# Optimization experiments

Measured on AMD Instinct MI355X. Metric: run time of the kernel, lower is better.

## Reference

```python
import jax, jax.numpy as jnp
import numpy as np
import math

FEATURE_DIMS = 6
D_HIDDEN = 32
N_TOKENS = 2097152
NUM_SEGMENTS = 8192
SCALE = 400.0 / math.log(10.0)


def setup_inputs() -> dict:
    key = jax.random.key(0)
    ks = jax.random.split(key, 8)
    x = jax.random.normal(ks[0], (N_TOKENS, FEATURE_DIMS), dtype=jnp.float32)
    segment_ids = jnp.sort(jax.random.randint(ks[1], (N_TOKENS,), 0, NUM_SEGMENTS)).astype(jnp.int32)
    # params (kaiming-ish init, same layout as nn.Linear: y = x @ W.T + b -> stored pre-transposed)
    W1 = jax.random.normal(ks[2], (FEATURE_DIMS, D_HIDDEN), dtype=jnp.float32) / np.sqrt(FEATURE_DIMS)
    b1 = jax.random.normal(ks[3], (D_HIDDEN,), dtype=jnp.float32) * 0.01
    wr = jax.random.normal(ks[4], (D_HIDDEN,), dtype=jnp.float32) / np.sqrt(D_HIDDEN)
    br = jax.random.normal(ks[5], (), dtype=jnp.float32) * 0.01
    wz = jax.random.normal(ks[6], (D_HIDDEN,), dtype=jnp.float32) / np.sqrt(D_HIDDEN)
    bz = jax.random.normal(ks[7], (), dtype=jnp.float32) * 0.01
    return {"x": x, "W1": W1, "b1": b1, "wr": wr, "br": br, "wz": wz, "bz": bz,
            "segment_ids": segment_ids, "num_segments": NUM_SEGMENTS}


def reference(x, W1, b1, wr, br, wz, bz, segment_ids, num_segments):
    # layer1: Linear + ReLU  -> h [N, d_hidden]
    h = jax.nn.relu(x @ W1 + b1)
    # rating / weight heads, squeezed to [N]
    r = h @ wr + br
    z = h @ wz + bz
    # per-segment (per-game) softmax over z, weighted sum of r -- single pass, no Python loop
    zmax = jax.ops.segment_max(z, segment_ids, num_segments=num_segments)  # [G], -inf for empty
    e = jnp.exp(z - zmax[segment_ids])                                      # [N]
    num = jax.ops.segment_sum(e * r, segment_ids, num_segments=num_segments)  # [G]
    den = jax.ops.segment_sum(e, segment_ids, num_segments=num_segments)      # [G]
    den_safe = jnp.where(den > 0, den, 1.0)
    preds = jnp.where(den > 0, num / den_safe, 0.0)  # empty segment -> 0, as in the torch code
    return SCALE * preds
```

## Files before the change

### kernel.cpp

```cpp
#include <hip/hip_runtime.h>

#define SCALE_F 173.71779276130078f
#define BLOCK 256
#define TPT 2
#define TOK_PER_BLOCK (BLOCK * TPT)

typedef float v2f __attribute__((ext_vector_type(2)));

__global__ void zero_ws_kernel(float* __restrict__ ws, int n) {
    int i = blockIdx.x * 256 + threadIdx.x;
    if (i < n) ws[i] = 0.0f;
}

__device__ __forceinline__ int swz(int q) { return q ^ ((q >> 3) & 7); }

__global__ __launch_bounds__(BLOCK, 8) void strength_main_kernel(
    const float* __restrict__ x,
    const float* __restrict__ W1,
    const float* __restrict__ b1,
    const float* __restrict__ wr,
    const float* __restrict__ brp,
    const float* __restrict__ wz,
    const float* __restrict__ bzp,
    const int*   __restrict__ seg,
    int N,
    float* __restrict__ num,
    float* __restrict__ den)
{
    __shared__ float4 xs[TOK_PER_BLOCK * 6 / 4];

    const int tid    = threadIdx.x;
    const int lane   = tid & 63;
    const int bstart = blockIdx.x * TOK_PER_BLOCK;
    const int t0     = bstart + tid * TPT;

    float a[TPT * 6];
    int   sg[TPT];
    int   kmax;

    if (bstart + TOK_PER_BLOCK <= N) {
        kmax = TPT;
        const float4* xg = (const float4*)(x + (size_t)bstart * 6);
        #pragma unroll
        for (int i = 0; i < 3; ++i) {
            int q = tid + BLOCK * i;
            xs[swz(q)] = xg[q];
        }
        __syncthreads();
        float4 v0 = xs[swz(3 * tid + 0)];
        float4 v1 = xs[swz(3 * tid + 1)];
        float4 v2 = xs[swz(3 * tid + 2)];
        a[0] = v0.x; a[1]  = v0.y; a[2]  = v0.z; a[3]  = v0.w;
        a[4] = v1.x; a[5]  = v1.y; a[6]  = v1.z; a[7]  = v1.w;
        a[8] = v2.x; a[9]  = v2.y; a[10] = v2.z; a[11] = v2.w;
        int2 s2 = *(const int2*)(seg + t0);
        sg[0] = s2.x; sg[1] = s2.y;
    } else {
        kmax = (t0 >= N) ? 0 : ((N - t0 < TPT) ? (N - t0) : TPT);
        #pragma unroll
        for (int k = 0; k < TPT; ++k) {
            if (k < kmax) {
                const float* xp = x + (size_t)(t0 + k) * 6;
                #pragma unroll
                for (int i = 0; i < 6; ++i) a[k * 6 + i] = xp[i];
                sg[k] = seg[t0 + k];
            } else {
                #pragma unroll
                for (int i = 0; i < 6; ++i) a[k * 6 + i] = 0.0f;
                sg[k] = -1;
            }
        }
    }

    v2f X[6];
    #pragma unroll
    for (int f = 0; f < 6; ++f) X[f] = (v2f){ a[f], a[6 + f] };

    const float brv = *brp;
    const float bzv = *bzp;

    v2f R = (v2f){brv, brv};
    v2f Z = (v2f){bzv, bzv};

    #pragma unroll 2
    for (int c = 0; c < 16; ++c) {
        const float2 w0 = *(const float2*)&W1[0 * 32 + 2 * c];
        const float2 w1 = *(const float2*)&W1[1 * 32 + 2 * c];
        const float2 w2 = *(const float2*)&W1[2 * 32 + 2 * c];
        const float2 w3 = *(const float2*)&W1[3 * 32 + 2 * c];
        const float2 w4 = *(const float2*)&W1[4 * 32 + 2 * c];
        const float2 w5 = *(const float2*)&W1[5 * 32 + 2 * c];
        const float2 bb = *(const float2*)&b1[2 * c];
        const float2 rr = *(const float2*)&wr[2 * c];
        const float2 zz = *(const float2*)&wz[2 * c];

        #pragma unroll
        for (int j = 0; j < 2; ++j) {
            const float wj0 = j ? w0.y : w0.x;
            const float wj1 = j ? w1.y : w1.x;
            const float wj2 = j ? w2.y : w2.x;
            const float wj3 = j ? w3.y : w3.x;
            const float wj4 = j ? w4.y : w4.x;
            const float wj5 = j ? w5.y : w5.x;
            const float bbj = j ? bb.y : bb.x;
            const float rrj = j ? rr.y : rr.x;
            const float zzj = j ? zz.y : zz.x;
            const v2f vw0 = (v2f){wj0, wj0}, vw1 = (v2f){wj1, wj1};
            const v2f vw2 = (v2f){wj2, wj2}, vw3 = (v2f){wj3, wj3};
            const v2f vw4 = (v2f){wj4, wj4}, vw5 = (v2f){wj5, wj5};
            const v2f vbb = (v2f){bbj, bbj};
            const v2f vrr = (v2f){rrj, rrj}, vzz = (v2f){zzj, zzj};
            v2f h = X[0]*vw0 + (X[1]*vw1 + (X[2]*vw2 +
                    (X[3]*vw3 + (X[4]*vw4 + (X[5]*vw5 + vbb)))));
            h = __builtin_elementwise_max(h, (v2f){0.f, 0.f});
            R = h * vrr + R;
            Z = h * vzz + Z;
        }
    }

    float rv[TPT] = { R.x, R.y };
    float zv[TPT] = { Z.x, Z.y };

    int   key = (kmax > 0) ? sg[0] : -1;
    float E = 0.0f, ER = 0.0f;
    #pragma unroll
    for (int k = 0; k < TPT; ++k) {
        if (k < kmax) {
            float e = __expf(zv[k]);
            if (sg[k] != key) {
                atomicAdd(&den[key], E);
                atomicAdd(&num[key], ER);
                key = sg[k]; E = 0.0f; ER = 0.0f;
            }
            E += e; ER = fmaf(e, rv[k], ER);
        }
    }

    #pragma unroll
    for (int d = 1; d < 64; d <<= 1) {
        int   k2 = __shfl_up(key, d);
        float E2 = __shfl_up(E,   d);
        float R2 = __shfl_up(ER,  d);
        if (lane >= d && k2 == key) { E += E2; ER += R2; }
    }
    int knext = __shfl_down(key, 1);
    bool last = (lane == 63) || (knext != key);
    if (last && key >= 0) {
        atomicAdd(&den[key], E);
        atomicAdd(&num[key], ER);
    }
}

__global__ void finalize_kernel(const float* __restrict__ num,
                                const float* __restrict__ den,
                                float* __restrict__ out, int G) {
    int g = blockIdx.x * 256 + threadIdx.x;
    if (g < G) {
        float d = den[g];
        out[g] = (d > 0.0f) ? (SCALE_F * num[g] / d) : 0.0f;
    }
}

extern "C" void kernel_launch(void* const* d_in, const int* in_sizes, int n_in,
                              void* d_out, int out_size, void* d_ws, size_t ws_size,
                              hipStream_t stream) {
    const float* x   = (const float*)d_in[0];
    const float* W1  = (const float*)d_in[1];
    const float* b1  = (const float*)d_in[2];
    const float* wr  = (const float*)d_in[3];
    const float* br  = (const float*)d_in[4];
    const float* wz  = (const float*)d_in[5];
    const float* bz  = (const float*)d_in[6];
    const int*   seg = (const int*)d_in[7];

    int N = in_sizes[7];
    int G = out_size;

    float* num = (float*)d_ws;
    float* den = num + G;
    float* out = (float*)d_out;

    int zn = 2 * G;
    zero_ws_kernel<<<(zn + 255) / 256, 256, 0, stream>>>(num, zn);

    int nblocks = (int)(((long)N + TOK_PER_BLOCK - 1) / TOK_PER_BLOCK);
    strength_main_kernel<<<nblocks, BLOCK, 0, stream>>>(
        x, W1, b1, wr, br, wz, bz, seg, N, num, den);

    finalize_kernel<<<(G + 255) / 256, 256, 0, stream>>>(num, den, out, G);
}
```

Baseline: 30.89 us.

## Drop LDS staging and process two grid-strided chunks per thread

Removes the shared-memory staging and barrier for x, so each thread loads its two tokens' features directly as three float4 reads. Each thread now handles two chunks spaced a grid-span apart, with both chunks' loads issued up front before any compute, which halves the block count. The direct per-thread float4 loads are less coalesced than the staged version, and more registers are live per thread, which may reduce occupancy.

```diff
diff --git a/kernel.cpp b/kernel.cpp
--- a/kernel.cpp
+++ b/kernel.cpp
@@ -3,7 +3,7 @@
 #define SCALE_F 173.71779276130078f
 #define BLOCK 256
 #define TPT 2
-#define TOK_PER_BLOCK (BLOCK * TPT)
+#define NCHUNK 2
 
 typedef float v2f __attribute__((ext_vector_type(2)));
 
@@ -11,8 +11,6 @@
     int i = blockIdx.x * 256 + threadIdx.x;
     if (i < n) ws[i] = 0.0f;
 }
-
-__device__ __forceinline__ int swz(int q) { return q ^ ((q >> 3) & 7); }
 
 __global__ __launch_bounds__(BLOCK, 8) void strength_main_kernel(
     const float* __restrict__ x,
@@ -27,127 +25,124 @@
     float* __restrict__ num,
     float* __restrict__ den)
 {
-    __shared__ float4 xs[TOK_PER_BLOCK * 6 / 4];
+    const int tid  = threadIdx.x;
+    const int lane = tid & 63;
+    const int span = gridDim.x * (BLOCK * TPT);
 
-    const int tid    = threadIdx.x;
-    const int lane   = tid & 63;
-    const int bstart = blockIdx.x * TOK_PER_BLOCK;
-    const int t0     = bstart + tid * TPT;
+    float a[NCHUNK][TPT * 6];
+    int   sg[NCHUNK][TPT];
+    int   kmax[NCHUNK];
+    int   t0c[NCHUNK];
 
-    float a[TPT * 6];
-    int   sg[TPT];
-    int   kmax;
-
-    if (bstart + TOK_PER_BLOCK <= N) {
-        kmax = TPT;
-        const float4* xg = (const float4*)(x + (size_t)bstart * 6);
-        #pragma unroll
-        for (int i = 0; i < 3; ++i) {
-            int q = tid + BLOCK * i;
-            xs[swz(q)] = xg[q];
-        }
-        __syncthreads();
-        float4 v0 = xs[swz(3 * tid + 0)];
-        float4 v1 = xs[swz(3 * tid + 1)];
-        float4 v2 = xs[swz(3 * tid + 2)];
-        a[0] = v0.x; a[1]  = v0.y; a[2]  = v0.z; a[3]  = v0.w;
-        a[4] = v1.x; a[5]  = v1.y; a[6]  = v1.z; a[7]  = v1.w;
-        a[8] = v2.x; a[9]  = v2.y; a[10] = v2.z; a[11] = v2.w;
-        int2 s2 = *(const int2*)(seg + t0);
-        sg[0] = s2.x; sg[1] = s2.y;
-    } else {
-        kmax = (t0 >= N) ? 0 : ((N - t0 < TPT) ? (N - t0) : TPT);
-        #pragma unroll
-        for (int k = 0; k < TPT; ++k) {
-            if (k < kmax) {
-                const float* xp = x + (size_t)(t0 + k) * 6;
-                #pragma unroll
-                for (int i = 0; i < 6; ++i) a[k * 6 + i] = xp[i];
-                sg[k] = seg[t0 + k];
-            } else {
-                #pragma unroll
-                for (int i = 0; i < 6; ++i) a[k * 6 + i] = 0.0f;
-                sg[k] = -1;
+    #pragma unroll
+    for (int c = 0; c < NCHUNK; ++c) {
+        const int t0 = blockIdx.x * (BLOCK * TPT) + c * span + tid * TPT;
+        t0c[c]  = t0;
+        kmax[c] = (t0 >= N) ? 0 : ((N - t0 < TPT) ? (N - t0) : TPT);
+        if (kmax[c] == TPT) {
+            const float4* xp = (const float4*)(x + (size_t)t0 * 6);
+            float4 v0 = xp[0], v1 = xp[1], v2 = xp[2];
+            a[c][0] = v0.x; a[c][1]  = v0.y; a[c][2]  = v0.z; a[c][3]  = v0.w;
+            a[c][4] = v1.x; a[c][5]  = v1.y; a[c][6]  = v1.z; a[c][7]  = v1.w;
+            a[c][8] = v2.x; a[c][9]  = v2.y; a[c][10] = v2.z; a[c][11] = v2.w;
+            int2 s2 = *(const int2*)(seg + t0);
+            sg[c][0] = s2.x; sg[c][1] = s2.y;
+        } else {
+            #pragma unroll
+            for (int k = 0; k < TPT; ++k) {
+                if (k < kmax[c]) {
+                    const float* xp = x + (size_t)(t0 + k) * 6;
+                    #pragma unroll
+                    for (int i = 0; i < 6; ++i) a[c][k * 6 + i] = xp[i];
+                    sg[c][k] = seg[t0 + k];
+                } else {
+                    #pragma unroll
+                    for (int i = 0; i < 6; ++i) a[c][k * 6 + i] = 0.0f;
+                    sg[c][k] = -1;
+                }
             }
         }
     }
 
-    v2f X[6];
-    #pragma unroll
-    for (int f = 0; f < 6; ++f) X[f] = (v2f){ a[f], a[6 + f] };
-
     const float brv = *brp;
     const float bzv = *bzp;
 
-    v2f R = (v2f){brv, brv};
-    v2f Z = (v2f){bzv, bzv};
+    #pragma unroll
+    for (int c = 0; c < NCHUNK; ++c) {
+        v2f X[6];
+        #pragma unroll
+        for (int f = 0; f < 6; ++f) X[f] = (v2f){ a[c][f], a[c][6 + f] };
 
-    #pragma unroll 2
-    for (int c = 0; c < 16; ++c) {
-        const float2 w0 = *(const float2*)&W1[0 * 32 + 2 * c];
-        const float2 w1 = *(const float2*)&W1[1 * 32 + 2 * c];
-        const float2 w2 = *(const float2*)&W1[2 * 32 + 2 * c];
-        const float2 w3 = *(const float2*)&W1[3 * 32 + 2 * c];
-        const float2 w4 = *(const float2*)&W1[4 * 32 + 2 * c];
-        const float2 w5 = *(const float2*)&W1[5 * 32 + 2 * c];
-        const float2 bb = *(const float2*)&b1[2 * c];
-        const float2 rr = *(const float2*)&wr[2 * c];
-        const float2 zz = *(const float2*)&wz[2 * c];
+        v2f R = (v2f){brv, brv};
+        v2f Z = (v2f){bzv, bzv};
+
+        #pragma unroll 2
+        for (int cc = 0; cc < 16; ++cc) {
+            const float2 w0 = *(const float2*)&W1[0 * 32 + 2 * cc];
+            const float2 w1 = *(const float2*)&W1[1 * 32 + 2 * cc];
+            const float2 w2 = *(const float2*)&W1[2 * 32 + 2 * cc];
+            const float2 w3 = *(const float2*)&W1[3 * 32 + 2 * cc];
+            const float2 w4 = *(const float2*)&W1[4 * 32 + 2 * cc];
+            const float2 w5 = *(const float2*)&W1[5 * 32 + 2 * cc];
+            const float2 bb = *(const float2*)&b1[2 * cc];
+            const float2 rr = *(const float2*)&wr[2 * cc];
+            const float2 zz = *(const float2*)&wz[2 * cc];
+
+            #pragma unroll
+            for (int j = 0; j < 2; ++j) {
+                const float wj0 = j ? w0.y : w0.x;
+                const float wj1 = j ? w1.y : w1.x;
+                const float wj2 = j ? w2.y : w2.x;
+                const float wj3 = j ? w3.y : w3.x;
+                const float wj4 = j ? w4.y : w4.x;
+                const float wj5 = j ? w5.y : w5.x;
+                const float bbj = j ? bb.y : bb.x;
+                const float rrj = j ? rr.y : rr.x;
+                const float zzj = j ? zz.y : zz.x;
+                const v2f vw0 = (v2f){wj0, wj0}, vw1 = (v2f){wj1, wj1};
+                const v2f vw2 = (v2f){wj2, wj2}, vw3 = (v2f){wj3, wj3};
+                const v2f vw4 = (v2f){wj4, wj4}, vw5 = (v2f){wj5, wj5};
+                const v2f vbb = (v2f){bbj, bbj};
+                const v2f vrr = (v2f){rrj, rrj}, vzz = (v2f){zzj, zzj};
+                v2f h = X[0]*vw0 + (X[1]*vw1 + (X[2]*vw2 +
+                        (X[3]*vw3 + (X[4]*vw4 + (X[5]*vw5 + vbb)))));
+                h = __builtin_elementwise_max(h, (v2f){0.f, 0.f});
+                R = h * vrr + R;
+                Z = h * vzz + Z;
+            }
+        }
+
+        float rv[TPT] = { R.x, R.y };
+        float zv[TPT] = { Z.x, Z.y };
+
+        int   key = (kmax[c] > 0) ? sg[c][0] : -1;
+        float E = 0.0f, ER = 0.0f;
+        #pragma unroll
+        for (int k = 0; k < TPT; ++k) {
+            if (k < kmax[c]) {
+                float e = __expf(zv[k]);
+                if (sg[c][k] != key) {
+                    atomicAdd(&den[key], E);
+                    atomicAdd(&num[key], ER);
+                    key = sg[c][k]; E = 0.0f; ER = 0.0f;
+                }
+                E += e; ER = fmaf(e, rv[k], ER);
+            }
+        }
 
         #pragma unroll
-        for (int j = 0; j < 2; ++j) {
-            const float wj0 = j ? w0.y : w0.x;
-            const float wj1 = j ? w1.y : w1.x;
-            const float wj2 = j ? w2.y : w2.x;
-            const float wj3 = j ? w3.y : w3.x;
-            const float wj4 = j ? w4.y : w4.x;
-            const float wj5 = j ? w5.y : w5.x;
-            const float bbj = j ? bb.y : bb.x;
-            const float rrj = j ? rr.y : rr.x;
-            const float zzj = j ? zz.y : zz.x;
-            const v2f vw0 = (v2f){wj0, wj0}, vw1 = (v2f){wj1, wj1};
-            const v2f vw2 = (v2f){wj2, wj2}, vw3 = (v2f){wj3, wj3};
-            const v2f vw4 = (v2f){wj4, wj4}, vw5 = (v2f){wj5, wj5};
-            const v2f vbb = (v2f){bbj, bbj};
-            const v2f vrr = (v2f){rrj, rrj}, vzz = (v2f){zzj, zzj};
-            v2f h = X[0]*vw0 + (X[1]*vw1 + (X[2]*vw2 +
-                    (X[3]*vw3 + (X[4]*vw4 + (X[5]*vw5 + vbb)))));
-            h = __builtin_elementwise_max(h, (v2f){0.f, 0.f});
-            R = h * vrr + R;
-            Z = h * vzz + Z;
+        for (int d = 1; d < 64; d <<= 1) {
+            int   k2 = __shfl_up(key, d);
+            float E2 = __shfl_up(E,   d);
+            float R2 = __shfl_up(ER,  d);
+            if (lane >= d && k2 == key) { E += E2; ER += R2; }
         }
-    }
-
-    float rv[TPT] = { R.x, R.y };
-    float zv[TPT] = { Z.x, Z.y };
-
-    int   key = (kmax > 0) ? sg[0] : -1;
-    float E = 0.0f, ER = 0.0f;
-    #pragma unroll
-    for (int k = 0; k < TPT; ++k) {
-        if (k < kmax) {
-            float e = __expf(zv[k]);
-            if (sg[k] != key) {
-                atomicAdd(&den[key], E);
-                atomicAdd(&num[key], ER);
-                key = sg[k]; E = 0.0f; ER = 0.0f;
-            }
-            E += e; ER = fmaf(e, rv[k], ER);
+        int  knext = __shfl_down(key, 1);
+        bool last  = (lane == 63) || (knext != key);
+        if (last && key >= 0) {
+            atomicAdd(&den[key], E);
+            atomicAdd(&num[key], ER);
         }
-    }
-
-    #pragma unroll
-    for (int d = 1; d < 64; d <<= 1) {
-        int   k2 = __shfl_up(key, d);
-        float E2 = __shfl_up(E,   d);
-        float R2 = __shfl_up(ER,  d);
-        if (lane >= d && k2 == key) { E += E2; ER += R2; }
-    }
-    int knext = __shfl_down(key, 1);
-    bool last = (lane == 63) || (knext != key);
-    if (last && key >= 0) {
-        atomicAdd(&den[key], E);
-        atomicAdd(&num[key], ER);
     }
 }
 
@@ -183,7 +178,8 @@
     int zn = 2 * G;
     zero_ws_kernel<<<(zn + 255) / 256, 256, 0, stream>>>(num, zn);
 
-    int nblocks = (int)(((long)N + TOK_PER_BLOCK - 1) / TOK_PER_BLOCK);
+    long tokens_per_block = (long)BLOCK * TPT * NCHUNK;
+    int  nblocks = (int)(((long)N + tokens_per_block - 1) / tokens_per_block);
     strength_main_kernel<<<nblocks, BLOCK, 0, stream>>>(
         x, W1, b1, wr, br, wz, bz, seg, N, num, den);
 
```

Measured after the change: 32.07 us. 3.8% more time.
